# Performance work log

Measured on AMD Instinct MI355X. Metric: run time of the kernel, lower is better.

The kernel has to match this reference:

```python
import jax, jax.numpy as jnp
import numpy as np

B, C, N, K = 16, 64, 2048, 20   # batch, in_channel, points, knn
T, O = 3, 64                    # taylor_channel, out_channel
EPS = 1e-5                      # torch BatchNorm2d default eps


def setup_inputs() -> dict:
    key = jax.random.key(0)
    ks = jax.random.split(key, 11)
    feat = jax.random.normal(ks[0], (B, C, N), jnp.float32)
    idx = jax.random.randint(ks[1], (B, N, K), 0, N, dtype=jnp.int32)
    group_pc = jax.random.normal(ks[2], (B, 3, N, K), jnp.float32) * 0.1
    # conv1: 1x1 conv 19 -> T, bias, no bn/activation
    W1 = jax.random.normal(ks[3], (T, 19), jnp.float32) * 0.1
    b1 = jax.random.normal(ks[4], (T,), jnp.float32) * 0.01
    # conv2: kernel [1,K], (C*T) -> O, bias, then BN(eval) + ReLU
    W2 = jax.random.normal(ks[5], (O, C * T, K), jnp.float32) * 0.02
    b2 = jax.random.normal(ks[6], (O,), jnp.float32) * 0.01
    gamma = 1.0 + 0.1 * jax.random.normal(ks[7], (O,), jnp.float32)
    beta = 0.1 * jax.random.normal(ks[8], (O,), jnp.float32)
    run_mean = 0.1 * jax.random.normal(ks[9], (O,), jnp.float32)
    run_var = jax.random.uniform(ks[10], (O,), jnp.float32, 0.5, 1.5)
    return {"feat": feat, "idx": idx, "group_pc": group_pc,
            "W1": W1, "b1": b1, "W2": W2, "b2": b2,
            "gamma": gamma, "beta": beta,
            "run_mean": run_mean, "run_var": run_var}


def _taylor_terms(group_pc):
    # group_pc: (B,3,N,K) -> 19 polynomial channels (B,19,N,K)
    X, Y, Z = group_pc[:, 0], group_pc[:, 1], group_pc[:, 2]
    XX, YY, ZZ = X * X, Y * Y, Z * Z
    XY, XZ, YZ = X * Y, X * Z, Y * Z
    terms = [X, Y, Z, XX, YY, ZZ, XX * X, YY * Y, ZZ * Z,
             XY, XZ, YZ, X * XY, X * XZ, Y * YZ, Y * XY,
             Z * XZ, Z * YZ, XY * Z]
    return jnp.stack(terms, axis=1)


def reference(feat, idx, group_pc, W1, b1, W2, b2, gamma, beta, run_mean, run_var):
    # KNN gather: feat (B,C,N), idx (B,N,K) -> (B,C,N,K)
    group_feat = jax.vmap(lambda f, i: f[:, i])(feat, idx)
    # Taylor polynomial features -> (B,19,N,K)
    gxyz = _taylor_terms(group_pc)
    # conv1 (1x1): (B,T,N,K)
    taylor = jnp.einsum('tc,bcnk->btnk', W1, gxyz) + b1[None, :, None, None]
    # outer product over channels: (B, C*T, N, K)
    prod = (group_feat[:, :, None] * taylor[:, None]).reshape(B, C * T, N, K)
    # conv2 kernel [1,K]: contract input channels and k -> (B,O,N)
    out = jnp.einsum('bink,oik->bon', prod, W2) + b2[None, :, None]
    # BatchNorm (eval mode) + ReLU
    inv = gamma / jnp.sqrt(run_var + EPS)
    out = (out - run_mean[None, :, None]) * inv[None, :, None] + beta[None, :, None]
    return jax.nn.relu(out)
```

## Files before the change

kernel.cpp:

```cpp
#include <hip/hip_runtime.h>

#define B_   16
#define C_   64
#define N_   2048
#define K_   20
#define O_   64
#define EPS_ 1e-5f

#define NT   32
#define RP   64
#define CT   (C_*3)

typedef float  f32x4 __attribute__((ext_vector_type(4)));
typedef short  s16x8 __attribute__((ext_vector_type(8)));

__device__ __forceinline__ unsigned short f2bf(float x) {
    union { float f; unsigned int u; } v; v.f = x;
    unsigned int r = (v.u + 0x7fffu + ((v.u >> 16) & 1u)) >> 16;
    return (unsigned short)r;
}

__global__ void prep_kernel(const float* __restrict__ W2,
                            const float* __restrict__ b2,
                            const float* __restrict__ gamma,
                            const float* __restrict__ beta,
                            const float* __restrict__ run_mean,
                            const float* __restrict__ run_var,
                            unsigned short* __restrict__ W2fb,
                            float* __restrict__ bias2) {
    int e = blockIdx.x * blockDim.x + threadIdx.x;
    const int total = C_ * O_ * RP;
    if (e < total) {
        int r = e & 63;
        int o = (e >> 6) & 63;
        int c = e >> 12;
        float v = 0.f;
        if (r < 60) {
            int t = r / K_, k = r % K_;
            float inv = gamma[o] * rsqrtf(run_var[o] + EPS_);
            v = W2[(o * CT + (c * 3 + t)) * K_ + k] * inv;
        }
        W2fb[e] = f2bf(v);
    } else if (e < total + O_) {
        int o = e - total;
        float inv = gamma[o] * rsqrtf(run_var[o] + EPS_);
        bias2[o] = (b2[o] - run_mean[o]) * inv + beta[o];
    }
}

__global__ __launch_bounds__(128) void spider_mfma(
    const float* __restrict__ feat,
    const int*   __restrict__ idx,
    const float* __restrict__ gpc,
    const float* __restrict__ W1,
    const float* __restrict__ b1,
    const unsigned short* __restrict__ W2fb,
    const float* __restrict__ bias2,
    float* __restrict__ out)
{
    __shared__ __align__(16) float          s_tay[60 * NT];
    __shared__ __align__(16) float          s_w1[60];
    __shared__ __align__(16) unsigned short s_W[O_ * RP];
    __shared__ __align__(16) unsigned short s_P[NT * RP];

    const int tid = threadIdx.x;
    const int b   = blockIdx.y;
    const int n0  = blockIdx.x * NT;
    const int pt  = tid & 31;
    const int grp = tid >> 5;
    const int k0  = grp * 5;
    const int w   = tid >> 6;
    const int l   = tid & 63;

    if (tid < 57)      s_w1[tid] = W1[tid];
    else if (tid < 60) s_w1[tid] = b1[tid - 57];
    if (tid < NT) {
        int addr = tid * 128 + ((7 ^ (tid & 7)) << 4) + 8;
        *(unsigned long long*)((char*)s_P + addr) = 0ull;
    }
    __syncthreads();

    {
        const float* pcb = gpc + ((size_t)b * 3 * N_ + (n0 + pt)) * K_;
        #pragma unroll
        for (int i = 0; i < 5; ++i) {
            int k = k0 + i;
            float X = pcb[k];
            float Y = pcb[(size_t)N_ * K_ + k];
            float Z = pcb[(size_t)2 * N_ * K_ + k];
            float XX = X * X, YY = Y * Y, ZZ = Z * Z;
            float XY = X * Y, XZ = X * Z, YZ = Y * Z;
            float tm[19] = {X, Y, Z, XX, YY, ZZ,
                            XX * X, YY * Y, ZZ * Z,
                            XY, XZ, YZ,
                            X * XY, X * XZ, Y * YZ,
                            Y * XY, Z * XZ, Z * YZ, XY * Z};
            #pragma unroll
            for (int t = 0; t < 3; ++t) {
                float a = s_w1[57 + t];
                #pragma unroll
                for (int j = 0; j < 19; ++j) a += s_w1[t * 19 + j] * tm[j];
                s_tay[(t * K_ + k) * NT + pt] = a;
            }
        }
    }

    int iv[5];
    {
        const int* ig = idx + ((size_t)b * N_ + n0 + pt) * K_ + k0;
        #pragma unroll
        for (int i = 0; i < 5; ++i) iv[i] = ig[i];
    }
    __syncthreads();

    f32x4 acc[2][2];
    #pragma unroll
    for (int mt = 0; mt < 2; ++mt)
        #pragma unroll
        for (int nt = 0; nt < 2; ++nt)
            acc[mt][nt] = (f32x4){0.f, 0.f, 0.f, 0.f};

    const float* featb = feat + (size_t)b * C_ * N_;

    for (int c = 0; c < C_; ++c) {
        const s16x8* wg = (const s16x8*)(W2fb + (size_t)c * (O_ * RP));
        #pragma unroll
        for (int q = 0; q < 4; ++q) {
            int s  = tid * 4 + q;
            int o  = s >> 3, kb = s & 7;
            s16x8 v = wg[s];
            *(s16x8*)((char*)s_W + o * 128 + ((kb ^ (o & 7)) << 4)) = v;
        }
        const float* fr = featb + (size_t)c * N_;
        #pragma unroll
        for (int i = 0; i < 5; ++i) {
            int k = k0 + i;
            float g = fr[iv[i]];
            #pragma unroll
            for (int t = 0; t < 3; ++t) {
                float p = g * s_tay[(t * K_ + k) * NT + pt];
                int byte = (t * K_ + k) * 2;
                int addr = pt * 128 + (((byte >> 4) ^ (pt & 7)) << 4) + (byte & 15);
                *(unsigned short*)((char*)s_P + addr) = f2bf(p);
            }
        }
        __syncthreads();

        #pragma unroll
        for (int ks = 0; ks < 2; ++ks) {
            int kb8 = ks * 4 + (l >> 4);
            int o0 = w * 32 + (l & 15);
            int o1 = o0 + 16;
            int p0 = (l & 15);
            int p1 = p0 + 16;
            s16x8 a0 = *(const s16x8*)((char*)s_W + o0 * 128 + ((kb8 ^ (o0 & 7)) << 4));
            s16x8 a1 = *(const s16x8*)((char*)s_W + o1 * 128 + ((kb8 ^ (o1 & 7)) << 4));
            s16x8 b0 = *(const s16x8*)((char*)s_P + p0 * 128 + ((kb8 ^ (p0 & 7)) << 4));
            s16x8 b1 = *(const s16x8*)((char*)s_P + p1 * 128 + ((kb8 ^ (p1 & 7)) << 4));
            acc[0][0] = __builtin_amdgcn_mfma_f32_16x16x32_bf16(a0, b0, acc[0][0], 0, 0, 0);
            acc[0][1] = __builtin_amdgcn_mfma_f32_16x16x32_bf16(a0, b1, acc[0][1], 0, 0, 0);
            acc[1][0] = __builtin_amdgcn_mfma_f32_16x16x32_bf16(a1, b0, acc[1][0], 0, 0, 0);
            acc[1][1] = __builtin_amdgcn_mfma_f32_16x16x32_bf16(a1, b1, acc[1][1], 0, 0, 0);
        }
        __syncthreads();
    }

    #pragma unroll
    for (int mt = 0; mt < 2; ++mt) {
        #pragma unroll
        for (int nt = 0; nt < 2; ++nt) {
            #pragma unroll
            for (int r = 0; r < 4; ++r) {
                int o = w * 32 + mt * 16 + (l >> 4) * 4 + r;
                int n = n0 + nt * 16 + (l & 15);
                float v = acc[mt][nt][r] + bias2[o];
                out[((size_t)b * O_ + o) * N_ + n] = fmaxf(v, 0.f);
            }
        }
    }
}

extern "C" void kernel_launch(void* const* d_in, const int* in_sizes, int n_in,
                              void* d_out, int out_size, void* d_ws, size_t ws_size,
                              hipStream_t stream) {
    const float* feat     = (const float*)d_in[0];
    const int*   idx      = (const int*)  d_in[1];
    const float* gpc      = (const float*)d_in[2];
    const float* W1       = (const float*)d_in[3];
    const float* b1       = (const float*)d_in[4];
    const float* W2       = (const float*)d_in[5];
    const float* b2       = (const float*)d_in[6];
    const float* gamma    = (const float*)d_in[7];
    const float* beta     = (const float*)d_in[8];
    const float* run_mean = (const float*)d_in[9];
    const float* run_var  = (const float*)d_in[10];
    float* out = (float*)d_out;

    unsigned short* W2fb = (unsigned short*)d_ws;
    float* bias2 = (float*)((char*)d_ws + (size_t)C_ * O_ * RP * 2);

    const int prep_total = C_ * O_ * RP + O_;
    prep_kernel<<<(prep_total + 255) / 256, 256, 0, stream>>>(
        W2, b2, gamma, beta, run_mean, run_var, W2fb, bias2);

    dim3 grid(N_ / NT, B_);
    spider_mfma<<<grid, 128, 0, stream>>>(
        feat, idx, gpc, W1, b1, W2fb, bias2, out);
}
```

Baseline: 154.2 us.

## Double-buffer W2 tiles via direct global-to-LDS loads and keep Taylor terms in registers

The prep kernel now writes W2 already in the XOR-swizzled LDS layout. The main loop can then prefetch the next channel's weight tile with global_load_lds straight into a second LDS buffer, overlapping it with the feature gather and MFMA work of the current channel. The Taylor coefficients stay in per-thread registers instead of an LDS array, which drops one barrier and the LDS reads in the product loop. The cost is double the weight LDS footprint, plus reliance on the barrier's implicit vmcnt wait to make the async LDS writes visible.

Result: slower. 167.2 us (+8.4%).

```diff
diff --git a/kernel.cpp b/kernel.cpp
--- a/kernel.cpp
+++ b/kernel.cpp
@@ -19,6 +19,11 @@
     unsigned int r = (v.u + 0x7fffu + ((v.u >> 16) & 1u)) >> 16;
     return (unsigned short)r;
 }
+
+#define GLD_LDS16(gsrc, ldst) \
+    __builtin_amdgcn_global_load_lds( \
+        (const __attribute__((address_space(1))) unsigned int*)(gsrc), \
+        (__attribute__((address_space(3)))       unsigned int*)(ldst), 16, 0, 0)
 
 __global__ void prep_kernel(const float* __restrict__ W2,
                             const float* __restrict__ b2,
@@ -40,7 +45,9 @@
             float inv = gamma[o] * rsqrtf(run_var[o] + EPS_);
             v = W2[(o * CT + (c * 3 + t)) * K_ + k] * inv;
         }
-        W2fb[e] = f2bf(v);
+        int kb = r >> 3, j = r & 7;
+        int slot = (o << 3) | (kb ^ (o & 7));
+        W2fb[((size_t)c << 12) | (slot << 3) | j] = f2bf(v);
     } else if (e < total + O_) {
         int o = e - total;
         float inv = gamma[o] * rsqrtf(run_var[o] + EPS_);
@@ -58,10 +65,9 @@
     const float* __restrict__ bias2,
     float* __restrict__ out)
 {
-    __shared__ __align__(16) float          s_tay[60 * NT];
-    __shared__ __align__(16) float          s_w1[60];
-    __shared__ __align__(16) unsigned short s_W[O_ * RP];
+    __shared__ __align__(16) unsigned short s_Wd[2][O_ * RP];
     __shared__ __align__(16) unsigned short s_P[NT * RP];
+    __shared__ __align__(16) float          s_w1[64];
 
     const int tid = threadIdx.x;
     const int b   = blockIdx.y;
@@ -78,8 +84,18 @@
         int addr = tid * 128 + ((7 ^ (tid & 7)) << 4) + 8;
         *(unsigned long long*)((char*)s_P + addr) = 0ull;
     }
+
+    {
+        const char* wsrc = (const char*)W2fb;
+        #pragma unroll
+        for (int q = 0; q < 4; ++q) {
+            int chunk = (w * 4 + q) * 1024;
+            GLD_LDS16(wsrc + chunk + l * 16, (char*)s_Wd[0] + chunk);
+        }
+    }
     __syncthreads();
 
+    float tayr[15];
     {
         const float* pcb = gpc + ((size_t)b * 3 * N_ + (n0 + pt)) * K_;
         #pragma unroll
@@ -100,7 +116,7 @@
                 float a = s_w1[57 + t];
                 #pragma unroll
                 for (int j = 0; j < 19; ++j) a += s_w1[t * 19 + j] * tm[j];
-                s_tay[(t * K_ + k) * NT + pt] = a;
+                tayr[t * 5 + i] = a;
             }
         }
     }
@@ -111,7 +127,6 @@
         #pragma unroll
         for (int i = 0; i < 5; ++i) iv[i] = ig[i];
     }
-    __syncthreads();
 
     f32x4 acc[2][2];
     #pragma unroll
@@ -123,14 +138,17 @@
     const float* featb = feat + (size_t)b * C_ * N_;
 
     for (int c = 0; c < C_; ++c) {
-        const s16x8* wg = (const s16x8*)(W2fb + (size_t)c * (O_ * RP));
-        #pragma unroll
-        for (int q = 0; q < 4; ++q) {
-            int s  = tid * 4 + q;
-            int o  = s >> 3, kb = s & 7;
-            s16x8 v = wg[s];
-            *(s16x8*)((char*)s_W + o * 128 + ((kb ^ (o & 7)) << 4)) = v;
-        }
+        const int cur = c & 1;
+
+        if (c < C_ - 1) {
+            const char* wsrc = (const char*)(W2fb + ((size_t)(c + 1) << 12));
+            #pragma unroll
+            for (int q = 0; q < 4; ++q) {
+                int chunk = (w * 4 + q) * 1024;
+                GLD_LDS16(wsrc + chunk + l * 16, (char*)s_Wd[cur ^ 1] + chunk);
+            }
+        }
+
         const float* fr = featb + (size_t)c * N_;
         #pragma unroll
         for (int i = 0; i < 5; ++i) {
@@ -138,7 +156,7 @@
             float g = fr[iv[i]];
             #pragma unroll
             for (int t = 0; t < 3; ++t) {
-                float p = g * s_tay[(t * K_ + k) * NT + pt];
+                float p = g * tayr[t * 5 + i];
                 int byte = (t * K_ + k) * 2;
                 int addr = pt * 128 + (((byte >> 4) ^ (pt & 7)) << 4) + (byte & 15);
                 *(unsigned short*)((char*)s_P + addr) = f2bf(p);
@@ -146,6 +164,7 @@
         }
         __syncthreads();
 
+        const unsigned short* sW = s_Wd[cur];
         #pragma unroll
         for (int ks = 0; ks < 2; ++ks) {
             int kb8 = ks * 4 + (l >> 4);
@@ -153,8 +172,8 @@
             int o1 = o0 + 16;
             int p0 = (l & 15);
             int p1 = p0 + 16;
-            s16x8 a0 = *(const s16x8*)((char*)s_W + o0 * 128 + ((kb8 ^ (o0 & 7)) << 4));
-            s16x8 a1 = *(const s16x8*)((char*)s_W + o1 * 128 + ((kb8 ^ (o1 & 7)) << 4));
+            s16x8 a0 = *(const s16x8*)((const char*)sW + o0 * 128 + ((kb8 ^ (o0 & 7)) << 4));
+            s16x8 a1 = *(const s16x8*)((const char*)sW + o1 * 128 + ((kb8 ^ (o1 & 7)) << 4));
             s16x8 b0 = *(const s16x8*)((char*)s_P + p0 * 128 + ((kb8 ^ (p0 & 7)) << 4));
             s16x8 b1 = *(const s16x8*)((char*)s_P + p1 * 128 + ((kb8 ^ (p1 & 7)) << 4));
             acc[0][0] = __builtin_amdgcn_mfma_f32_16x16x32_bf16(a0, b0, acc[0][0], 0, 0, 0);
```

## Single-wave blocks with register-resident W2 fragments and double-buffered LDS pipeline

Applied to the files above, without the earlier changes.

Each block now runs one 64-thread wave that handles all 64 output channels. W2 is pre-swizzled by the prep kernel into MFMA fragment order so it can be loaded straight into registers instead of staged through LDS. The gathered feature products are written into a double-buffered LDS tile while the next channel's gathers and weight loads are issued early, and the Taylor terms stay in registers. This removes the per-channel __syncthreads and LDS weight staging, but it raises register pressure and halves the threads per block, which may reduce occupancy and latency hiding.

Result: faster. 145.1 us (-5.9%).

```diff
diff --git a/kernel.cpp b/kernel.cpp
--- a/kernel.cpp
+++ b/kernel.cpp
@@ -8,16 +8,17 @@
 #define EPS_ 1e-5f
 
 #define NT   32
-#define RP   64
 #define CT   (C_*3)
 
-typedef float  f32x4 __attribute__((ext_vector_type(4)));
-typedef short  s16x8 __attribute__((ext_vector_type(8)));
+typedef float f32x4 __attribute__((ext_vector_type(4)));
+typedef short s16x8 __attribute__((ext_vector_type(8)));
 
 __device__ __forceinline__ unsigned short f2bf(float x) {
     union { float f; unsigned int u; } v; v.f = x;
-    unsigned int r = (v.u + 0x7fffu + ((v.u >> 16) & 1u)) >> 16;
-    return (unsigned short)r;
+    return (unsigned short)((v.u + 0x7fffu + ((v.u >> 16) & 1u)) >> 16);
+}
+__device__ __forceinline__ unsigned int pack2bf(float a, float b) {
+    return (unsigned int)f2bf(a) | ((unsigned int)f2bf(b) << 16);
 }
 
 __global__ void prep_kernel(const float* __restrict__ W2,
@@ -29,11 +30,15 @@
                             unsigned short* __restrict__ W2fb,
                             float* __restrict__ bias2) {
     int e = blockIdx.x * blockDim.x + threadIdx.x;
-    const int total = C_ * O_ * RP;
+    const int total = C_ * 8 * 64 * 8;
     if (e < total) {
-        int r = e & 63;
-        int o = (e >> 6) & 63;
-        int c = e >> 12;
+        int j  = e & 7;
+        int l  = (e >> 3) & 63;
+        int f  = (e >> 9) & 7;
+        int c  = e >> 12;
+        int ot = f >> 1, ks = f & 1;
+        int o  = ot * 16 + (l & 15);
+        int r  = ks * 32 + ((l >> 4) << 3) + j;
         float v = 0.f;
         if (r < 60) {
             int t = r / K_, k = r % K_;
@@ -48,7 +53,7 @@
     }
 }
 
-__global__ __launch_bounds__(128) void spider_mfma(
+__global__ __launch_bounds__(64) void spider_mfma(
     const float* __restrict__ feat,
     const int*   __restrict__ idx,
     const float* __restrict__ gpc,
@@ -58,36 +63,30 @@
     const float* __restrict__ bias2,
     float* __restrict__ out)
 {
-    __shared__ __align__(16) float          s_tay[60 * NT];
-    __shared__ __align__(16) float          s_w1[60];
-    __shared__ __align__(16) unsigned short s_W[O_ * RP];
-    __shared__ __align__(16) unsigned short s_P[NT * RP];
+    __shared__ __align__(16) char sP[2][NT * 128];
 
     const int tid = threadIdx.x;
     const int b   = blockIdx.y;
     const int n0  = blockIdx.x * NT;
     const int pt  = tid & 31;
     const int grp = tid >> 5;
-    const int k0  = grp * 5;
-    const int w   = tid >> 6;
-    const int l   = tid & 63;
-
-    if (tid < 57)      s_w1[tid] = W1[tid];
-    else if (tid < 60) s_w1[tid] = b1[tid - 57];
-    if (tid < NT) {
-        int addr = tid * 128 + ((7 ^ (tid & 7)) << 4) + 8;
-        *(unsigned long long*)((char*)s_P + addr) = 0ull;
-    }
-    __syncthreads();
-
+    const int l   = tid;
+
+    *(unsigned long long*)(sP[tid >> 5] + (tid & 31) * 128 +
+                           ((7 ^ (tid & 7)) << 4) + 8) = 0ull;
+
+    float tayr[30];
+    int   iv[10];
     {
-        const float* pcb = gpc + ((size_t)b * 3 * N_ + (n0 + pt)) * K_;
-        #pragma unroll
-        for (int i = 0; i < 5; ++i) {
-            int k = k0 + i;
-            float X = pcb[k];
-            float Y = pcb[(size_t)N_ * K_ + k];
-            float Z = pcb[(size_t)2 * N_ * K_ + k];
+        const int k0 = grp * 10;
+        const float* pcb = gpc + ((size_t)b * 3 * N_ + (n0 + pt)) * K_ + k0;
+        const int*   ig  = idx + ((size_t)b * N_ + (n0 + pt)) * K_ + k0;
+        #pragma unroll
+        for (int q = 0; q < 10; ++q) {
+            iv[q] = ig[q];
+            float X = pcb[q];
+            float Y = pcb[N_ * K_ + q];
+            float Z = pcb[2 * N_ * K_ + q];
             float XX = X * X, YY = Y * Y, ZZ = Z * Z;
             float XY = X * Y, XZ = X * Z, YZ = Y * Z;
             float tm[19] = {X, Y, Z, XX, YY, ZZ,
@@ -97,83 +96,89 @@
                             Y * XY, Z * XZ, Z * YZ, XY * Z};
             #pragma unroll
             for (int t = 0; t < 3; ++t) {
-                float a = s_w1[57 + t];
+                float a = b1[t];
                 #pragma unroll
-                for (int j = 0; j < 19; ++j) a += s_w1[t * 19 + j] * tm[j];
-                s_tay[(t * K_ + k) * NT + pt] = a;
-            }
-        }
-    }
-
-    int iv[5];
-    {
-        const int* ig = idx + ((size_t)b * N_ + n0 + pt) * K_ + k0;
-        #pragma unroll
-        for (int i = 0; i < 5; ++i) iv[i] = ig[i];
-    }
-    __syncthreads();
-
-    f32x4 acc[2][2];
+                for (int j = 0; j < 19; ++j) a += W1[t * 19 + j] * tm[j];
+                tayr[t * 10 + q] = a;
+            }
+        }
+    }
+
+    const s16x8* Wfrag = (const s16x8*)W2fb;
+    const float* featb = feat + (size_t)b * C_ * N_;
+
+    s16x8 wA[8], wB[8];
+    float gA[10], gB[10];
+    f32x4 acc[4][2];
     #pragma unroll
-    for (int mt = 0; mt < 2; ++mt)
-        #pragma unroll
-        for (int nt = 0; nt < 2; ++nt)
-            acc[mt][nt] = (f32x4){0.f, 0.f, 0.f, 0.f};
-
-    const float* featb = feat + (size_t)b * C_ * N_;
-
-    for (int c = 0; c < C_; ++c) {
-        const s16x8* wg = (const s16x8*)(W2fb + (size_t)c * (O_ * RP));
-        #pragma unroll
-        for (int q = 0; q < 4; ++q) {
-            int s  = tid * 4 + q;
-            int o  = s >> 3, kb = s & 7;
-            s16x8 v = wg[s];
-            *(s16x8*)((char*)s_W + o * 128 + ((kb ^ (o & 7)) << 4)) = v;
-        }
-        const float* fr = featb + (size_t)c * N_;
-        #pragma unroll
-        for (int i = 0; i < 5; ++i) {
-            int k = k0 + i;
-            float g = fr[iv[i]];
-            #pragma unroll
-            for (int t = 0; t < 3; ++t) {
-                float p = g * s_tay[(t * K_ + k) * NT + pt];
-                int byte = (t * K_ + k) * 2;
-                int addr = pt * 128 + (((byte >> 4) ^ (pt & 7)) << 4) + (byte & 15);
-                *(unsigned short*)((char*)s_P + addr) = f2bf(p);
-            }
-        }
-        __syncthreads();
-
+    for (int ot = 0; ot < 4; ++ot)
+        #pragma unroll
+        for (int p = 0; p < 2; ++p) acc[ot][p] = (f32x4){0.f, 0.f, 0.f, 0.f};
+
+    auto issueW = [&](s16x8 (&w)[8], int cc) {
+        const s16x8* p = Wfrag + (size_t)cc * 512 + l;
+        #pragma unroll
+        for (int f = 0; f < 8; ++f) w[f] = p[f * 64];
+    };
+    auto issueG = [&](float (&g)[10], int cc) {
+        const float* fr = featb + (size_t)cc * N_;
+        #pragma unroll
+        for (int q = 0; q < 10; ++q) g[q] = fr[iv[q]];
+    };
+    auto writeP = [&](int buf, float (&g)[10]) {
+        char* base = sP[buf] + pt * 128;
+        #pragma unroll
+        for (int t = 0; t < 3; ++t) {
+            #pragma unroll
+            for (int i = 0; i < 5; ++i) {
+                int byte = t * 40 + grp * 20 + i * 4;
+                unsigned int v = pack2bf(g[2 * i]     * tayr[t * 10 + 2 * i],
+                                         g[2 * i + 1] * tayr[t * 10 + 2 * i + 1]);
+                *(unsigned int*)(base + ((((byte >> 4) ^ (pt & 7))) << 4) + (byte & 15)) = v;
+            }
+        }
+    };
+    auto mfmaC = [&](s16x8 (&w)[8], int buf) {
         #pragma unroll
         for (int ks = 0; ks < 2; ++ks) {
             int kb8 = ks * 4 + (l >> 4);
-            int o0 = w * 32 + (l & 15);
-            int o1 = o0 + 16;
-            int p0 = (l & 15);
-            int p1 = p0 + 16;
-            s16x8 a0 = *(const s16x8*)((char*)s_W + o0 * 128 + ((kb8 ^ (o0 & 7)) << 4));
-            s16x8 a1 = *(const s16x8*)((char*)s_W + o1 * 128 + ((kb8 ^ (o1 & 7)) << 4));
-            s16x8 b0 = *(const s16x8*)((char*)s_P + p0 * 128 + ((kb8 ^ (p0 & 7)) << 4));
-            s16x8 b1 = *(const s16x8*)((char*)s_P + p1 * 128 + ((kb8 ^ (p1 & 7)) << 4));
-            acc[0][0] = __builtin_amdgcn_mfma_f32_16x16x32_bf16(a0, b0, acc[0][0], 0, 0, 0);
-            acc[0][1] = __builtin_amdgcn_mfma_f32_16x16x32_bf16(a0, b1, acc[0][1], 0, 0, 0);
-            acc[1][0] = __builtin_amdgcn_mfma_f32_16x16x32_bf16(a1, b0, acc[1][0], 0, 0, 0);
-            acc[1][1] = __builtin_amdgcn_mfma_f32_16x16x32_bf16(a1, b1, acc[1][1], 0, 0, 0);
-        }
-        __syncthreads();
+            #pragma unroll
+            for (int pti = 0; pti < 2; ++pti) {
+                int p = pti * 16 + (l & 15);
+                s16x8 bf = *(const s16x8*)(sP[buf] + p * 128 + ((kb8 ^ (p & 7)) << 4));
+                #pragma unroll
+                for (int ot = 0; ot < 4; ++ot)
+                    acc[ot][pti] = __builtin_amdgcn_mfma_f32_16x16x32_bf16(
+                        w[ot * 2 + ks], bf, acc[ot][pti], 0, 0, 0);
+            }
+        }
+    };
+
+    issueG(gA, 0); issueW(wA, 0);
+    writeP(0, gA);
+    issueG(gB, 1); issueW(wB, 1);
+
+    for (int c = 0; c < C_; c += 2) {
+        mfmaC(wA, 0);
+        writeP(1, gB);
+        int c2 = (c + 2 < C_) ? c + 2 : C_ - 1;
+        issueG(gA, c2); issueW(wA, c2);
+        mfmaC(wB, 1);
+        writeP(0, gA);
+        int c3 = (c + 3 < C_) ? c + 3 : C_ - 1;
+        issueG(gB, c3); issueW(wB, c3);
     }
 
     #pragma unroll
-    for (int mt = 0; mt < 2; ++mt) {
-        #pragma unroll
-        for (int nt = 0; nt < 2; ++nt) {
+    for (int ot = 0; ot < 4; ++ot) {
+        f32x4 bv = *(const f32x4*)&bias2[ot * 16 + (l >> 4) * 4];
+        #pragma unroll
+        for (int pti = 0; pti < 2; ++pti) {
             #pragma unroll
             for (int r = 0; r < 4; ++r) {
-                int o = w * 32 + mt * 16 + (l >> 4) * 4 + r;
-                int n = n0 + nt * 16 + (l & 15);
-                float v = acc[mt][nt][r] + bias2[o];
+                int o = ot * 16 + (l >> 4) * 4 + r;
+                int n = n0 + pti * 16 + (l & 15);
+                float v = acc[ot][pti][r] + bv[r];
                 out[((size_t)b * O_ + o) * N_ + n] = fmaxf(v, 0.f);
             }
         }
@@ -197,13 +202,13 @@
     float* out = (float*)d_out;
 
     unsigned short* W2fb = (unsigned short*)d_ws;
-    float* bias2 = (float*)((char*)d_ws + (size_t)C_ * O_ * RP * 2);
-
-    const int prep_total = C_ * O_ * RP + O_;
+    float* bias2 = (float*)((char*)d_ws + (size_t)C_ * 8 * 64 * 8 * 2);
+
+    const int prep_total = C_ * 8 * 64 * 8 + O_;
     prep_kernel<<<(prep_total + 255) / 256, 256, 0, stream>>>(
         W2, b2, gamma, beta, run_mean, run_var, W2fb, bias2);
 
     dim3 grid(N_ / NT, B_);
-    spider_mfma<<<grid, 128, 0, stream>>>(
+    spider_mfma<<<grid, 64, 0, stream>>>(
         feat, idx, gpc, W1, b1, W2fb, bias2, out);
 }
```
